# Kernel tuning notes

Measured on AMD Instinct MI355X. Metric: run time of the kernel, lower is better.

The kernel has to match this reference:

```python
import jax, jax.numpy as jnp
import numpy as np

NUM_LEVELS = 16
BASE_RES = 16
MAX_RES = 2048
TABLE_SIZE = 1 << 19
FEATS = 2
GROWTH = np.exp((np.log(MAX_RES) - np.log(BASE_RES)) / (NUM_LEVELS - 1))
SCALINGS = jnp.asarray(np.floor(BASE_RES * GROWTH ** np.arange(NUM_LEVELS)), dtype=jnp.float32)  # [L]
OFFSETS = jnp.arange(NUM_LEVELS, dtype=jnp.int32) * TABLE_SIZE  # per-level slice offset into table
AABB_MIN, AABB_MAX = -1.0, 1.0
P1, P2 = jnp.uint32(2654435761), jnp.uint32(805459861)
MASK = jnp.uint32(TABLE_SIZE - 1)


def sh16(d):
    # spherical harmonics components, levels=4 -> 16 components (nerfstudio convention)
    x, y, z = d[..., 0], d[..., 1], d[..., 2]
    xx, yy, zz = x * x, y * y, z * z
    return jnp.stack([
        jnp.full_like(x, 0.28209479177387814),
        -0.48860251190291987 * y,
        0.48860251190291987 * z,
        -0.48860251190291987 * x,
        1.0925484305920792 * x * y,
        -1.0925484305920792 * y * z,
        0.94617469575755997 * zz - 0.31539156525251999,
        -1.0925484305920792 * x * z,
        0.54627421529603959 * (xx - yy),
        0.59004358992664352 * y * (3.0 * xx - yy),
        2.8906114426405538 * x * y * z,
        0.45704579946446572 * y * (5.0 * zz - 1.0),
        0.37317633259011546 * z * (5.0 * zz - 3.0),
        0.45704579946446572 * x * (5.0 * zz - 1.0),
        1.4453057213202769 * z * (xx - yy),
        0.59004358992664352 * x * (xx - 3.0 * yy),
    ], axis=-1)


def hash_fn(x, y, z):
    # spatial hash with wraparound uint32 arithmetic; lower 19 bits match int64 math mod 2^19
    v = x ^ (y * P1) ^ (z * P2)
    return (v & MASK).astype(jnp.int32) + OFFSETS  # [N, L]


def hash_encode(pts, table):
    # pts: [N,3] in [0,1]; table: [L*T, F]
    scaled = pts[:, None, :] * SCALINGS[None, :, None]  # [N, L, 3]
    f = jnp.floor(scaled)
    c = jnp.ceil(scaled)
    off = scaled - f  # [N, L, 3]
    fi = f.astype(jnp.uint32)
    ci = c.astype(jnp.uint32)
    cx, cy, cz = ci[..., 0], ci[..., 1], ci[..., 2]
    fx, fy, fz = fi[..., 0], fi[..., 1], fi[..., 2]
    # corner order matches nerfstudio hashed_0..7
    idx = jnp.stack([
        hash_fn(cx, cy, cz), hash_fn(cx, fy, cz), hash_fn(fx, fy, cz), hash_fn(fx, cy, cz),
        hash_fn(cx, cy, fz), hash_fn(cx, fy, fz), hash_fn(fx, fy, fz), hash_fn(fx, cy, fz),
    ], axis=0)  # [8, N, L]
    feats = table[idx]  # [8, N, L, F]
    ox, oy, oz = off[..., 0:1], off[..., 1:2], off[..., 2:3]
    f03 = feats[0] * ox + feats[3] * (1.0 - ox)
    f12 = feats[1] * ox + feats[2] * (1.0 - ox)
    f56 = feats[5] * ox + feats[6] * (1.0 - ox)
    f47 = feats[4] * ox + feats[7] * (1.0 - ox)
    f0312 = f03 * oy + f12 * (1.0 - oy)
    f4756 = f47 * oy + f56 * (1.0 - oy)
    enc = f0312 * oz + f4756 * (1.0 - oz)  # [N, L, F]
    return enc.reshape(enc.shape[0], NUM_LEVELS * FEATS)


def setup_inputs() -> dict:
    key = jax.random.key(0)
    ks = jax.random.split(key, 16)
    B, S = 4096, 48
    positions = jax.random.uniform(ks[0], (B, S, 3), jnp.float32) * 2.0 - 1.0
    densities = jax.random.normal(ks[1], (B, S, 1), jnp.float32)
    normals = jax.random.normal(ks[2], (B, 3), jnp.float32)
    camera_to_worlds = jax.random.normal(ks[3], (B, 3, 4), jnp.float32) * 0.3
    hash_table = (jax.random.uniform(ks[4], (NUM_LEVELS * TABLE_SIZE, FEATS), jnp.float32) * 2.0 - 1.0) * 1e-4
    def lin(k, i, o):
        return jax.random.normal(k, (i, o), jnp.float32) * (1.0 / np.sqrt(i))
    return {
        'positions': positions, 'densities': densities, 'normals': normals,
        'camera_to_worlds': camera_to_worlds, 'hash_table': hash_table,
        'w1': lin(ks[5], 32, 64), 'b1': jnp.zeros((64,), jnp.float32),
        'w2': lin(ks[6], 64, 16), 'b2': jnp.zeros((16,), jnp.float32),
        'h1': lin(ks[7], 32, 64), 'hb1': jnp.zeros((64,), jnp.float32),
        'h2': lin(ks[8], 64, 64), 'hb2': jnp.zeros((64,), jnp.float32),
        'h3': lin(ks[9], 64, 3), 'hb3': jnp.zeros((3,), jnp.float32),
    }


def reference(positions, densities, normals, camera_to_worlds, hash_table,
              w1, b1, w2, b2, h1, hb1, h2, hb2, h3, hb3):
    B, S, _ = positions.shape
    R = camera_to_worlds[..., :3, :3]
    t = camera_to_worlds[..., :3, 3]
    Rinv = jnp.swapaxes(R, -1, -2)  # pose inverse for rigid transform
    tinv = -jnp.einsum('bij,bj->bi', Rinv, t)
    pos = jnp.einsum('bij,bsj->bsi', Rinv, positions) + tinv[:, None, :]  # world -> camera
    pos = (pos - AABB_MIN) / (AABB_MAX - AABB_MIN)  # SceneBox.get_normalized_positions
    n_cam = jnp.einsum('bij,bj->bi', Rinv, normals)
    n_cam = (n_cam + 1.0) / 2.0  # get_normalized_directions
    d = sh16(n_cam)  # [B, 16]
    d = jnp.broadcast_to(d[:, None, :], (B, S, 16)).reshape(-1, 16)
    selector = jnp.all((pos > 0.0) & (pos < 1.0), axis=-1)
    pos = pos * selector[..., None]
    enc = hash_encode(pos.reshape(-1, 3), hash_table)  # [B*S, 32]
    geo = jax.nn.relu(jax.nn.relu(enc @ w1 + b1) @ w2 + b2)  # mlp_base, out ReLU
    h = jnp.concatenate([d, geo], axis=-1)  # [B*S, 32]
    rgb = jax.nn.sigmoid(jax.nn.relu(jax.nn.relu(h @ h1 + hb1) @ h2 + hb2) @ h3 + hb3)
    rgb = rgb.reshape(B, S, 3)
    weight = jax.nn.softmax(densities, axis=-2)  # softmax over samples
    return jnp.sum(weight * rgb, axis=-2)  # [B, 3] == FieldHeadNames.RGB_AFFINE
```

## Files before the change

### kernel.cpp

```cpp
#include <hip/hip_runtime.h>
#include <math.h>
#include <stdint.h>

#define NLEV 16
#define TSIZE (1u << 19)
#define NB 4096
#define NS 48
#define NPTS (NB * NS)

typedef __attribute__((ext_vector_type(8))) short short8;
typedef __attribute__((ext_vector_type(4))) float f32x4;

struct Scales { float s[NLEV]; };

__device__ __forceinline__ uint32_t hash3(uint32_t x, uint32_t y, uint32_t z) {
    return (x ^ (y * 2654435761u) ^ (z * 805459861u)) & (TSIZE - 1u);
}

__device__ __forceinline__ float sigmoidf(float v) {
    return 1.0f / (1.0f + expf(-v));
}

__device__ __forceinline__ ushort f2b(float f) {
    union { float f; uint32_t u; } v; v.f = f;
    uint32_t r = (v.u + 0x7FFFu + ((v.u >> 16) & 1u)) >> 16;
    return (ushort)r;
}

#define MFMA16(a, b, c) __builtin_amdgcn_mfma_f32_16x16x32_bf16((a), (b), (c), 0, 0, 0)

__global__ __launch_bounds__(256) void prep_kernel(
    const float* __restrict__ w1, const float* __restrict__ w2,
    const float* __restrict__ h1, const float* __restrict__ h2,
    const float* __restrict__ h3,
    ushort* __restrict__ bank)
{
    for (int idx = threadIdx.x; idx < 20 * 512; idx += 256) {
        const int f    = idx >> 9;
        const int r    = idx & 511;
        const int lane = r >> 3;
        const int j    = r & 7;
        const int l15  = lane & 15;
        const int quad = lane >> 4;
        const int k8   = quad * 8 + j;
        float val;
        if (f < 4) {
            val = w1[k8 * 64 + f * 16 + l15];
        } else if (f < 6) {
            val = w2[((f - 4) * 32 + k8) * 16 + l15];
        } else if (f < 10) {
            val = h1[k8 * 64 + (f - 6) * 16 + l15];
        } else if (f < 18) {
            const int t = f - 10, nt = t >> 1, kk = t & 1;
            val = h2[(kk * 32 + k8) * 64 + nt * 16 + l15];
        } else {
            val = (l15 < 3) ? h3[((f - 18) * 32 + k8) * 3 + l15] : 0.0f;
        }
        bank[idx] = f2b(val);
    }
}

__global__ __launch_bounds__(256) void encode_kernel(
    const float* __restrict__ positions,
    const float* __restrict__ c2w,
    const float* __restrict__ table,
    uint32_t* __restrict__ enc_ws,
    Scales sc)
{
    const int p = blockIdx.x * blockDim.x + threadIdx.x;
    if (p >= NPTS) return;
    const int l = blockIdx.y;
    const int b = p / NS;

    const float* M = c2w + b * 12;
    const float px = positions[3 * p + 0];
    const float py = positions[3 * p + 1];
    const float pz = positions[3 * p + 2];
    const float dx = px - M[3], dy = py - M[7], dz = pz - M[11];
    float qx = M[0] * dx + M[4] * dy + M[8] * dz;
    float qy = M[1] * dx + M[5] * dy + M[9] * dz;
    float qz = M[2] * dx + M[6] * dy + M[10] * dz;
    qx = (qx + 1.0f) * 0.5f;
    qy = (qy + 1.0f) * 0.5f;
    qz = (qz + 1.0f) * 0.5f;
    const bool sel = (qx > 0.0f) && (qx < 1.0f) &&
                     (qy > 0.0f) && (qy < 1.0f) &&
                     (qz > 0.0f) && (qz < 1.0f);
    if (!sel) { qx = 0.0f; qy = 0.0f; qz = 0.0f; }

    const float s = sc.s[l];
    const float sx = qx * s, sy = qy * s, sz = qz * s;
    const float fx = floorf(sx), fy = floorf(sy), fz = floorf(sz);
    const float cx = ceilf(sx),  cy = ceilf(sy),  cz = ceilf(sz);
    const float ox = sx - fx, oy = sy - fy, oz = sz - fz;
    const uint32_t fxi = (uint32_t)fx, fyi = (uint32_t)fy, fzi = (uint32_t)fz;
    const uint32_t cxi = (uint32_t)cx, cyi = (uint32_t)cy, czi = (uint32_t)cz;

    const float2* tab2 = (const float2*)table + (uint32_t)l * TSIZE;
    const float2 f0 = tab2[hash3(cxi, cyi, czi)];
    const float2 f1 = tab2[hash3(cxi, fyi, czi)];
    const float2 f2 = tab2[hash3(fxi, fyi, czi)];
    const float2 f3 = tab2[hash3(fxi, cyi, czi)];
    const float2 f4 = tab2[hash3(cxi, cyi, fzi)];
    const float2 f5 = tab2[hash3(cxi, fyi, fzi)];
    const float2 f6 = tab2[hash3(fxi, fyi, fzi)];
    const float2 f7 = tab2[hash3(fxi, cyi, fzi)];

    const float omx = 1.0f - ox, omy = 1.0f - oy, omz = 1.0f - oz;
    float f03x = f0.x * ox + f3.x * omx, f03y = f0.y * ox + f3.y * omx;
    float f12x = f1.x * ox + f2.x * omx, f12y = f1.y * ox + f2.y * omx;
    float f56x = f5.x * ox + f6.x * omx, f56y = f5.y * ox + f6.y * omx;
    float f47x = f4.x * ox + f7.x * omx, f47y = f4.y * ox + f7.y * omx;
    float ax = f03x * oy + f12x * omy, ay = f03y * oy + f12y * omy;
    float bx = f47x * oy + f56x * omy, by = f47y * oy + f56y * omy;
    const float ex = ax * oz + bx * omz;
    const float ey = ay * oz + by * omz;
    enc_ws[l * NPTS + p] = ((uint32_t)f2b(ey) << 16) | (uint32_t)f2b(ex);
}

__global__ __launch_bounds__(256) void mfma_mlp_kernel(
    const uint32_t* __restrict__ enc_ws,
    const float* __restrict__ normals,
    const float* __restrict__ c2w,
    const ushort* __restrict__ bank,
    const float* __restrict__ b1, const float* __restrict__ b2,
    const float* __restrict__ hb1, const float* __restrict__ hb2,
    const float* __restrict__ hb3,
    float* __restrict__ rgb_out)
{
    __shared__ ushort sX[64 * 40];
    __shared__ ushort sA1[64 * 72];
    __shared__ ushort sHIN[64 * 40];
    __shared__ ushort sU[64 * 72];

    const int tid = threadIdx.x;
    const int p0  = blockIdx.x * 64;

    {
        const int pt = tid & 63;
        const int l0 = (tid >> 6) * 4;
        const int p  = p0 + pt;
#pragma unroll
        for (int l = l0; l < l0 + 4; ++l) {
            *(uint32_t*)&sX[pt * 40 + 2 * l] = enc_ws[l * NPTS + p];
        }
    }

    if (tid < 64) {
        const int p = p0 + tid;
        const int b = p / NS;
        const float* M = c2w + b * 12;
        const float n0 = normals[3 * b + 0];
        const float n1 = normals[3 * b + 1];
        const float n2 = normals[3 * b + 2];
        float x = M[0] * n0 + M[4] * n1 + M[8] * n2;
        float y = M[1] * n0 + M[5] * n1 + M[9] * n2;
        float z = M[2] * n0 + M[6] * n1 + M[10] * n2;
        x = (x + 1.0f) * 0.5f;
        y = (y + 1.0f) * 0.5f;
        z = (z + 1.0f) * 0.5f;
        const float xx = x * x, yy = y * y, zz = z * z;
        float sh[16];
        sh[0]  = 0.28209479177387814f;
        sh[1]  = -0.48860251190291987f * y;
        sh[2]  = 0.48860251190291987f * z;
        sh[3]  = -0.48860251190291987f * x;
        sh[4]  = 1.0925484305920792f * x * y;
        sh[5]  = -1.0925484305920792f * y * z;
        sh[6]  = 0.94617469575756f * zz - 0.31539156525252f;
        sh[7]  = -1.0925484305920792f * x * z;
        sh[8]  = 0.5462742152960396f * (xx - yy);
        sh[9]  = 0.5900435899266435f * y * (3.0f * xx - yy);
        sh[10] = 2.890611442640554f * x * y * z;
        sh[11] = 0.4570457994644657f * y * (5.0f * zz - 1.0f);
        sh[12] = 0.37317633259011546f * z * (5.0f * zz - 3.0f);
        sh[13] = 0.4570457994644657f * x * (5.0f * zz - 1.0f);
        sh[14] = 1.445305721320277f * z * (xx - yy);
        sh[15] = 0.5900435899266435f * x * (xx - 3.0f * yy);
#pragma unroll
        for (int i = 0; i < 16; ++i) sHIN[tid * 40 + i] = f2b(sh[i]);
    }

    const int lane = tid & 63;
    const int wv   = tid >> 6;
    const int l15  = lane & 15;
    const int quad = lane >> 4;
    float b1v[4], hb1v[4], hb2v[4];
#pragma unroll
    for (int nt = 0; nt < 4; ++nt) {
        b1v[nt]  = b1[nt * 16 + l15];
        hb1v[nt] = hb1[nt * 16 + l15];
        hb2v[nt] = hb2[nt * 16 + l15];
    }
    const float b2v  = b2[l15];
    const float hb3v = (l15 < 3) ? hb3[l15] : 0.0f;

    const ushort* fb = bank + lane * 8;
#define FRAG(f) (*(const short8*)(fb + (f) * 512))

    __syncthreads();

    const int arow  = wv * 16 + l15;
    const int crow0 = wv * 16 + quad * 4;
    const f32x4 zero = {0.0f, 0.0f, 0.0f, 0.0f};

    {
        const short8 a = *(const short8*)&sX[arow * 40 + quad * 8];
        f32x4 c[4];
#pragma unroll
        for (int nt = 0; nt < 4; ++nt) c[nt] = MFMA16(a, FRAG(nt), zero);
#pragma unroll
        for (int nt = 0; nt < 4; ++nt)
#pragma unroll
            for (int r = 0; r < 4; ++r) {
                const float v = fmaxf(c[nt][r] + b1v[nt], 0.0f);
                sA1[(crow0 + r) * 72 + nt * 16 + l15] = f2b(v);
            }
    }

    {
        const short8 a0 = *(const short8*)&sA1[arow * 72 + quad * 8];
        const short8 a1 = *(const short8*)&sA1[arow * 72 + 32 + quad * 8];
        f32x4 c = MFMA16(a0, FRAG(4), zero);
        c = MFMA16(a1, FRAG(5), c);
#pragma unroll
        for (int r = 0; r < 4; ++r) {
            const float v = fmaxf(c[r] + b2v, 0.0f);
            sHIN[(crow0 + r) * 40 + 16 + l15] = f2b(v);
        }
    }

    {
        const short8 a = *(const short8*)&sHIN[arow * 40 + quad * 8];
        f32x4 c[4];
#pragma unroll
        for (int nt = 0; nt < 4; ++nt) c[nt] = MFMA16(a, FRAG(6 + nt), zero);
#pragma unroll
        for (int nt = 0; nt < 4; ++nt)
#pragma unroll
            for (int r = 0; r < 4; ++r) {
                const float v = fmaxf(c[nt][r] + hb1v[nt], 0.0f);
                sU[(crow0 + r) * 72 + nt * 16 + l15] = f2b(v);
            }
    }

    {
        const short8 a0 = *(const short8*)&sU[arow * 72 + quad * 8];
        const short8 a1 = *(const short8*)&sU[arow * 72 + 32 + quad * 8];
        f32x4 c[4];
#pragma unroll
        for (int nt = 0; nt < 4; ++nt) {
            f32x4 t = MFMA16(a0, FRAG(10 + nt * 2), zero);
            c[nt] = MFMA16(a1, FRAG(11 + nt * 2), t);
        }
#pragma unroll
        for (int nt = 0; nt < 4; ++nt)
#pragma unroll
            for (int r = 0; r < 4; ++r) {
                const float v = fmaxf(c[nt][r] + hb2v[nt], 0.0f);
                sA1[(crow0 + r) * 72 + nt * 16 + l15] = f2b(v);
            }
    }

    {
        const short8 a0 = *(const short8*)&sA1[arow * 72 + quad * 8];
        const short8 a1 = *(const short8*)&sA1[arow * 72 + 32 + quad * 8];
        f32x4 c = MFMA16(a0, FRAG(18), zero);
        c = MFMA16(a1, FRAG(19), c);
        if (l15 < 3) {
#pragma unroll
            for (int r = 0; r < 4; ++r) {
                rgb_out[3 * (p0 + crow0 + r) + l15] = sigmoidf(c[r] + hb3v);
            }
        }
    }
#undef FRAG
}

__global__ __launch_bounds__(64) void reduce_kernel(
    const float* __restrict__ densities,
    const float* __restrict__ rgb,
    float* __restrict__ out)
{
    const int b = blockIdx.x;
    const int t = threadIdx.x;
    const bool valid = t < NS;

    float d = valid ? densities[b * NS + t] : -INFINITY;
    float m = d;
#pragma unroll
    for (int off = 32; off > 0; off >>= 1) m = fmaxf(m, __shfl_xor(m, off));
    float e = valid ? expf(d - m) : 0.0f;
    float sum = e;
#pragma unroll
    for (int off = 32; off > 0; off >>= 1) sum += __shfl_xor(sum, off);
    const float w = e / sum;

    float r0 = 0.0f, r1 = 0.0f, r2 = 0.0f;
    if (valid) {
        const int base = (b * NS + t) * 3;
        r0 = w * rgb[base + 0];
        r1 = w * rgb[base + 1];
        r2 = w * rgb[base + 2];
    }
#pragma unroll
    for (int off = 32; off > 0; off >>= 1) {
        r0 += __shfl_xor(r0, off);
        r1 += __shfl_xor(r1, off);
        r2 += __shfl_xor(r2, off);
    }
    if (t == 0) {
        out[3 * b + 0] = r0;
        out[3 * b + 1] = r1;
        out[3 * b + 2] = r2;
    }
}

extern "C" void kernel_launch(void* const* d_in, const int* in_sizes, int n_in,
                              void* d_out, int out_size, void* d_ws, size_t ws_size,
                              hipStream_t stream) {
    const float* positions = (const float*)d_in[0];
    const float* densities = (const float*)d_in[1];
    const float* normals   = (const float*)d_in[2];
    const float* c2w       = (const float*)d_in[3];
    const float* table     = (const float*)d_in[4];
    const float* w1  = (const float*)d_in[5];
    const float* b1  = (const float*)d_in[6];
    const float* w2  = (const float*)d_in[7];
    const float* b2  = (const float*)d_in[8];
    const float* h1  = (const float*)d_in[9];
    const float* hb1 = (const float*)d_in[10];
    const float* h2  = (const float*)d_in[11];
    const float* hb2 = (const float*)d_in[12];
    const float* h3  = (const float*)d_in[13];
    const float* hb3 = (const float*)d_in[14];
    float* out = (float*)d_out;

    ushort*   bank   = (ushort*)d_ws;
    uint32_t* enc_ws = (uint32_t*)((char*)d_ws + 20 * 1024);
    float*    rgb_ws = (float*)((char*)enc_ws + sizeof(uint32_t) * NLEV * NPTS);

    Scales sc;
    const double growth = exp((log(2048.0) - log(16.0)) / 15.0);
    for (int i = 0; i < NLEV; ++i)
        sc.s[i] = (float)floor(16.0 * pow(growth, (double)i));

    const int threads = 256;
    const int pblocks = NPTS / threads;

    prep_kernel<<<1, threads, 0, stream>>>(w1, w2, h1, h2, h3, bank);
    encode_kernel<<<dim3(pblocks, NLEV), threads, 0, stream>>>(
        positions, c2w, table, enc_ws, sc);
    mfma_mlp_kernel<<<NPTS / 64, threads, 0, stream>>>(
        enc_ws, normals, c2w, bank, b1, b2, hb1, hb2, hb3, rgb_ws);
    reduce_kernel<<<NB, 64, 0, stream>>>(densities, rgb_ws, out);
}
```

Measured before the change: 222.5 us.

## Fuse hash encoding into MLP kernel, dropping encoding workspace round-trip

Merges the per-level hash-grid encode kernel into the MFMA MLP kernel. Each block transforms its 64 points once into shared memory, then four waves each gather four levels and write packed bf16 features straight into the shared input tile. This removes the global write and re-read of the 16-level encoding buffer and one kernel launch. The cost is lower gather parallelism per block (4 levels per thread, run serially), fewer waves in flight to hide random table-lookup latency, and extra block-wide barriers between MLP stages.

Result: slower. 274.7 us (+23.4%).

```diff
diff --git a/kernel.cpp b/kernel.cpp
--- a/kernel.cpp
+++ b/kernel.cpp
@@ -60,74 +60,19 @@
     }
 }
 
-__global__ __launch_bounds__(256) void encode_kernel(
+__global__ __launch_bounds__(256) void fused_kernel(
     const float* __restrict__ positions,
+    const float* __restrict__ normals,
     const float* __restrict__ c2w,
     const float* __restrict__ table,
-    uint32_t* __restrict__ enc_ws,
-    Scales sc)
-{
-    const int p = blockIdx.x * blockDim.x + threadIdx.x;
-    if (p >= NPTS) return;
-    const int l = blockIdx.y;
-    const int b = p / NS;
-
-    const float* M = c2w + b * 12;
-    const float px = positions[3 * p + 0];
-    const float py = positions[3 * p + 1];
-    const float pz = positions[3 * p + 2];
-    const float dx = px - M[3], dy = py - M[7], dz = pz - M[11];
-    float qx = M[0] * dx + M[4] * dy + M[8] * dz;
-    float qy = M[1] * dx + M[5] * dy + M[9] * dz;
-    float qz = M[2] * dx + M[6] * dy + M[10] * dz;
-    qx = (qx + 1.0f) * 0.5f;
-    qy = (qy + 1.0f) * 0.5f;
-    qz = (qz + 1.0f) * 0.5f;
-    const bool sel = (qx > 0.0f) && (qx < 1.0f) &&
-                     (qy > 0.0f) && (qy < 1.0f) &&
-                     (qz > 0.0f) && (qz < 1.0f);
-    if (!sel) { qx = 0.0f; qy = 0.0f; qz = 0.0f; }
-
-    const float s = sc.s[l];
-    const float sx = qx * s, sy = qy * s, sz = qz * s;
-    const float fx = floorf(sx), fy = floorf(sy), fz = floorf(sz);
-    const float cx = ceilf(sx),  cy = ceilf(sy),  cz = ceilf(sz);
-    const float ox = sx - fx, oy = sy - fy, oz = sz - fz;
-    const uint32_t fxi = (uint32_t)fx, fyi = (uint32_t)fy, fzi = (uint32_t)fz;
-    const uint32_t cxi = (uint32_t)cx, cyi = (uint32_t)cy, czi = (uint32_t)cz;
-
-    const float2* tab2 = (const float2*)table + (uint32_t)l * TSIZE;
-    const float2 f0 = tab2[hash3(cxi, cyi, czi)];
-    const float2 f1 = tab2[hash3(cxi, fyi, czi)];
-    const float2 f2 = tab2[hash3(fxi, fyi, czi)];
-    const float2 f3 = tab2[hash3(fxi, cyi, czi)];
-    const float2 f4 = tab2[hash3(cxi, cyi, fzi)];
-    const float2 f5 = tab2[hash3(cxi, fyi, fzi)];
-    const float2 f6 = tab2[hash3(fxi, fyi, fzi)];
-    const float2 f7 = tab2[hash3(fxi, cyi, fzi)];
-
-    const float omx = 1.0f - ox, omy = 1.0f - oy, omz = 1.0f - oz;
-    float f03x = f0.x * ox + f3.x * omx, f03y = f0.y * ox + f3.y * omx;
-    float f12x = f1.x * ox + f2.x * omx, f12y = f1.y * ox + f2.y * omx;
-    float f56x = f5.x * ox + f6.x * omx, f56y = f5.y * ox + f6.y * omx;
-    float f47x = f4.x * ox + f7.x * omx, f47y = f4.y * ox + f7.y * omx;
-    float ax = f03x * oy + f12x * omy, ay = f03y * oy + f12y * omy;
-    float bx = f47x * oy + f56x * omy, by = f47y * oy + f56y * omy;
-    const float ex = ax * oz + bx * omz;
-    const float ey = ay * oz + by * omz;
-    enc_ws[l * NPTS + p] = ((uint32_t)f2b(ey) << 16) | (uint32_t)f2b(ex);
-}
-
-__global__ __launch_bounds__(256) void mfma_mlp_kernel(
-    const uint32_t* __restrict__ enc_ws,
-    const float* __restrict__ normals,
-    const float* __restrict__ c2w,
     const ushort* __restrict__ bank,
     const float* __restrict__ b1, const float* __restrict__ b2,
     const float* __restrict__ hb1, const float* __restrict__ hb2,
     const float* __restrict__ hb3,
-    float* __restrict__ rgb_out)
+    float* __restrict__ rgb_out,
+    Scales sc)
 {
+    __shared__ float4 sQ[64];
     __shared__ ushort sX[64 * 40];
     __shared__ ushort sA1[64 * 72];
     __shared__ ushort sHIN[64 * 40];
@@ -136,20 +81,26 @@
     const int tid = threadIdx.x;
     const int p0  = blockIdx.x * 64;
 
-    {
-        const int pt = tid & 63;
-        const int l0 = (tid >> 6) * 4;
-        const int p  = p0 + pt;
-#pragma unroll
-        for (int l = l0; l < l0 + 4; ++l) {
-            *(uint32_t*)&sX[pt * 40 + 2 * l] = enc_ws[l * NPTS + p];
-        }
-    }
-
     if (tid < 64) {
         const int p = p0 + tid;
         const int b = p / NS;
         const float* M = c2w + b * 12;
+        const float px = positions[3 * p + 0];
+        const float py = positions[3 * p + 1];
+        const float pz = positions[3 * p + 2];
+        const float dx = px - M[3], dy = py - M[7], dz = pz - M[11];
+        float qx = M[0] * dx + M[4] * dy + M[8] * dz;
+        float qy = M[1] * dx + M[5] * dy + M[9] * dz;
+        float qz = M[2] * dx + M[6] * dy + M[10] * dz;
+        qx = (qx + 1.0f) * 0.5f;
+        qy = (qy + 1.0f) * 0.5f;
+        qz = (qz + 1.0f) * 0.5f;
+        const bool sel = (qx > 0.0f) && (qx < 1.0f) &&
+                         (qy > 0.0f) && (qy < 1.0f) &&
+                         (qz > 0.0f) && (qz < 1.0f);
+        if (!sel) { qx = 0.0f; qy = 0.0f; qz = 0.0f; }
+        sQ[tid] = make_float4(qx, qy, qz, 0.0f);
+
         const float n0 = normals[3 * b + 0];
         const float n1 = normals[3 * b + 1];
         const float n2 = normals[3 * b + 2];
@@ -180,6 +131,46 @@
 #pragma unroll
         for (int i = 0; i < 16; ++i) sHIN[tid * 40 + i] = f2b(sh[i]);
     }
+    __syncthreads();
+
+    {
+        const int pt = tid & 63;
+        const int wv4 = tid >> 6;
+        const float4 q = sQ[pt];
+#pragma unroll
+        for (int i = 0; i < 4; ++i) {
+            const int l = i * 4 + wv4;
+            const float s = sc.s[l];
+            const float sx = q.x * s, sy = q.y * s, sz = q.z * s;
+            const float fx = floorf(sx), fy = floorf(sy), fz = floorf(sz);
+            const float cx = ceilf(sx),  cy = ceilf(sy),  cz = ceilf(sz);
+            const float ox = sx - fx, oy = sy - fy, oz = sz - fz;
+            const uint32_t fxi = (uint32_t)fx, fyi = (uint32_t)fy, fzi = (uint32_t)fz;
+            const uint32_t cxi = (uint32_t)cx, cyi = (uint32_t)cy, czi = (uint32_t)cz;
+
+            const float2* tab2 = (const float2*)table + (uint32_t)l * TSIZE;
+            const float2 f0 = tab2[hash3(cxi, cyi, czi)];
+            const float2 f1 = tab2[hash3(cxi, fyi, czi)];
+            const float2 f2 = tab2[hash3(fxi, fyi, czi)];
+            const float2 f3 = tab2[hash3(fxi, cyi, czi)];
+            const float2 f4 = tab2[hash3(cxi, cyi, fzi)];
+            const float2 f5 = tab2[hash3(cxi, fyi, fzi)];
+            const float2 f6 = tab2[hash3(fxi, fyi, fzi)];
+            const float2 f7 = tab2[hash3(fxi, cyi, fzi)];
+
+            const float omx = 1.0f - ox, omy = 1.0f - oy, omz = 1.0f - oz;
+            float f03x = f0.x * ox + f3.x * omx, f03y = f0.y * ox + f3.y * omx;
+            float f12x = f1.x * ox + f2.x * omx, f12y = f1.y * ox + f2.y * omx;
+            float f56x = f5.x * ox + f6.x * omx, f56y = f5.y * ox + f6.y * omx;
+            float f47x = f4.x * ox + f7.x * omx, f47y = f4.y * ox + f7.y * omx;
+            float ax = f03x * oy + f12x * omy, ay = f03y * oy + f12y * omy;
+            float bx = f47x * oy + f56x * omy, by = f47y * oy + f56y * omy;
+            const float ex = ax * oz + bx * omz;
+            const float ey = ay * oz + by * omz;
+            *(uint32_t*)&sX[pt * 40 + 2 * l] =
+                ((uint32_t)f2b(ey) << 16) | (uint32_t)f2b(ex);
+        }
+    }
 
     const int lane = tid & 63;
     const int wv   = tid >> 6;
@@ -217,6 +208,7 @@
                 sA1[(crow0 + r) * 72 + nt * 16 + l15] = f2b(v);
             }
     }
+    __syncthreads();
 
     {
         const short8 a0 = *(const short8*)&sA1[arow * 72 + quad * 8];
@@ -229,6 +221,7 @@
             sHIN[(crow0 + r) * 40 + 16 + l15] = f2b(v);
         }
     }
+    __syncthreads();
 
     {
         const short8 a = *(const short8*)&sHIN[arow * 40 + quad * 8];
@@ -243,6 +236,7 @@
                 sU[(crow0 + r) * 72 + nt * 16 + l15] = f2b(v);
             }
     }
+    __syncthreads();
 
     {
         const short8 a0 = *(const short8*)&sU[arow * 72 + quad * 8];
@@ -253,6 +247,7 @@
             f32x4 t = MFMA16(a0, FRAG(10 + nt * 2), zero);
             c[nt] = MFMA16(a1, FRAG(11 + nt * 2), t);
         }
+        __syncthreads();
 #pragma unroll
         for (int nt = 0; nt < 4; ++nt)
 #pragma unroll
@@ -261,6 +256,7 @@
                 sA1[(crow0 + r) * 72 + nt * 16 + l15] = f2b(v);
             }
     }
+    __syncthreads();
 
     {
         const short8 a0 = *(const short8*)&sA1[arow * 72 + quad * 8];
@@ -336,22 +332,17 @@
     const float* hb3 = (const float*)d_in[14];
     float* out = (float*)d_out;
 
-    ushort*   bank   = (ushort*)d_ws;
-    uint32_t* enc_ws = (uint32_t*)((char*)d_ws + 20 * 1024);
-    float*    rgb_ws = (float*)((char*)enc_ws + sizeof(uint32_t) * NLEV * NPTS);
+    ushort* bank   = (ushort*)d_ws;
+    float*  rgb_ws = (float*)((char*)d_ws + 20 * 1024);
 
     Scales sc;
     const double growth = exp((log(2048.0) - log(16.0)) / 15.0);
     for (int i = 0; i < NLEV; ++i)
         sc.s[i] = (float)floor(16.0 * pow(growth, (double)i));
 
-    const int threads = 256;
-    const int pblocks = NPTS / threads;
-
-    prep_kernel<<<1, threads, 0, stream>>>(w1, w2, h1, h2, h3, bank);
-    encode_kernel<<<dim3(pblocks, NLEV), threads, 0, stream>>>(
-        positions, c2w, table, enc_ws, sc);
-    mfma_mlp_kernel<<<NPTS / 64, threads, 0, stream>>>(
-        enc_ws, normals, c2w, bank, b1, b2, hb1, hb2, hb3, rgb_ws);
+    prep_kernel<<<1, 256, 0, stream>>>(w1, w2, h1, h2, h3, bank);
+    fused_kernel<<<NPTS / 64, 256, 0, stream>>>(
+        positions, normals, c2w, table, bank,
+        b1, b2, hb1, hb2, hb3, rgb_ws, sc);
     reduce_kernel<<<NB, 64, 0, stream>>>(densities, rgb_ws, out);
 }
```

## Convert hash table to packed bf16 and interleave levels in encode grid

Applied to the files above, without the earlier changes.

Adds a conversion pass in the prep kernel that packs the fp32 hash table into 4-byte bf16 pairs, then gathers from that smaller table in the encode kernel, halving the bytes per random gather. The encode grid is flattened so consecutive blocks cover different levels of the same points, which changes cache locality. Extra __syncthreads are inserted in the MLP kernel between shared-memory stages. The conversion reads and writes the whole 64 MB table on every call, which may cost more than the gathers save, and it reduces table precision.

After: 238.2 us. +7.0%, slower.

```diff
diff --git a/kernel.cpp b/kernel.cpp
--- a/kernel.cpp
+++ b/kernel.cpp
@@ -27,95 +27,153 @@
     return (ushort)r;
 }
 
+__device__ __forceinline__ float blo(uint32_t v) {
+    union { uint32_t u; float f; } t; t.u = v << 16; return t.f;
+}
+__device__ __forceinline__ float bhi(uint32_t v) {
+    union { uint32_t u; float f; } t; t.u = v & 0xFFFF0000u; return t.f;
+}
+
 #define MFMA16(a, b, c) __builtin_amdgcn_mfma_f32_16x16x32_bf16((a), (b), (c), 0, 0, 0)
 
 __global__ __launch_bounds__(256) void prep_kernel(
     const float* __restrict__ w1, const float* __restrict__ w2,
     const float* __restrict__ h1, const float* __restrict__ h2,
     const float* __restrict__ h3,
-    ushort* __restrict__ bank)
+    const float* __restrict__ table,
+    ushort* __restrict__ bank,
+    uint32_t* __restrict__ tb16)
 {
-    for (int idx = threadIdx.x; idx < 20 * 512; idx += 256) {
-        const int f    = idx >> 9;
-        const int r    = idx & 511;
-        const int lane = r >> 3;
-        const int j    = r & 7;
-        const int l15  = lane & 15;
-        const int quad = lane >> 4;
-        const int k8   = quad * 8 + j;
-        float val;
-        if (f < 4) {
-            val = w1[k8 * 64 + f * 16 + l15];
-        } else if (f < 6) {
-            val = w2[((f - 4) * 32 + k8) * 16 + l15];
-        } else if (f < 10) {
-            val = h1[k8 * 64 + (f - 6) * 16 + l15];
-        } else if (f < 18) {
-            const int t = f - 10, nt = t >> 1, kk = t & 1;
-            val = h2[(kk * 32 + k8) * 64 + nt * 16 + l15];
-        } else {
-            val = (l15 < 3) ? h3[((f - 18) * 32 + k8) * 3 + l15] : 0.0f;
-        }
-        bank[idx] = f2b(val);
-    }
-}
-
-__global__ __launch_bounds__(256) void encode_kernel(
+    if (blockIdx.x == 0) {
+        for (int idx = threadIdx.x; idx < 20 * 512; idx += 256) {
+            const int f    = idx >> 9;
+            const int r    = idx & 511;
+            const int lane = r >> 3;
+            const int j    = r & 7;
+            const int l15  = lane & 15;
+            const int quad = lane >> 4;
+            const int k8   = quad * 8 + j;
+            float val;
+            if (f < 4) {
+                val = w1[k8 * 64 + f * 16 + l15];
+            } else if (f < 6) {
+                val = w2[((f - 4) * 32 + k8) * 16 + l15];
+            } else if (f < 10) {
+                val = h1[k8 * 64 + (f - 6) * 16 + l15];
+            } else if (f < 18) {
+                const int t = f - 10, nt = t >> 1, kk = t & 1;
+                val = h2[(kk * 32 + k8) * 64 + nt * 16 + l15];
+            } else {
+                val = (l15 < 3) ? h3[((f - 18) * 32 + k8) * 3 + l15] : 0.0f;
+            }
+            bank[idx] = f2b(val);
+        }
+    }
+    if (tb16) {
+        const float2* t2 = (const float2*)table;
+        const int n = NLEV * TSIZE;
+        for (int i = blockIdx.x * blockDim.x + threadIdx.x; i < n;
+             i += gridDim.x * blockDim.x) {
+            const float2 e = t2[i];
+            tb16[i] = ((uint32_t)f2b(e.y) << 16) | (uint32_t)f2b(e.x);
+        }
+    }
+}
+
+#define ENCODE_PROLOG()                                                       \
+    const int bid = blockIdx.x;                                               \
+    const int l   = bid & 15;                         \
+    const int p   = (bid >> 4) * 256 + threadIdx.x;                           \
+    const int b   = p / NS;                                                   \
+    const float* M = c2w + b * 12;                                            \
+    const float px = positions[3 * p + 0];                                    \
+    const float py = positions[3 * p + 1];                                    \
+    const float pz = positions[3 * p + 2];                                    \
+    const float dx = px - M[3], dy = py - M[7], dz = pz - M[11];              \
+    float qx = M[0] * dx + M[4] * dy + M[8] * dz;                             \
+    float qy = M[1] * dx + M[5] * dy + M[9] * dz;                             \
+    float qz = M[2] * dx + M[6] * dy + M[10] * dz;                            \
+    qx = (qx + 1.0f) * 0.5f;                                                  \
+    qy = (qy + 1.0f) * 0.5f;                                                  \
+    qz = (qz + 1.0f) * 0.5f;                                                  \
+    const bool sel = (qx > 0.0f) && (qx < 1.0f) &&                            \
+                     (qy > 0.0f) && (qy < 1.0f) &&                            \
+                     (qz > 0.0f) && (qz < 1.0f);                              \
+    if (!sel) { qx = 0.0f; qy = 0.0f; qz = 0.0f; }                            \
+    const float s = sc.s[l];                                                  \
+    const float sx = qx * s, sy = qy * s, sz = qz * s;                        \
+    const float fx = floorf(sx), fy = floorf(sy), fz = floorf(sz);            \
+    const float cx = ceilf(sx),  cy = ceilf(sy),  cz = ceilf(sz);             \
+    const float ox = sx - fx, oy = sy - fy, oz = sz - fz;                     \
+    const uint32_t fxi = (uint32_t)fx, fyi = (uint32_t)fy, fzi = (uint32_t)fz;\
+    const uint32_t cxi = (uint32_t)cx, cyi = (uint32_t)cy, czi = (uint32_t)cz;
+
+#define ENCODE_EPILOG()                                                       \
+    const float omx = 1.0f - ox, omy = 1.0f - oy, omz = 1.0f - oz;            \
+    float f03x = f0x * ox + f3x * omx, f03y = f0y * ox + f3y * omx;           \
+    float f12x = f1x * ox + f2x * omx, f12y = f1y * ox + f2y * omx;           \
+    float f56x = f5x * ox + f6x * omx, f56y = f5y * ox + f6y * omx;           \
+    float f47x = f4x * ox + f7x * omx, f47y = f4y * ox + f7y * omx;           \
+    float ax = f03x * oy + f12x * omy, ay = f03y * oy + f12y * omy;           \
+    float bx = f47x * oy + f56x * omy, by = f47y * oy + f56y * omy;           \
+    const float ex = ax * oz + bx * omz;                                      \
+    const float ey = ay * oz + by * omz;                                      \
+    enc_ws[l * NPTS + p] = ((uint32_t)f2b(ey) << 16) | (uint32_t)f2b(ex);
+
+__global__ __launch_bounds__(256) void encode_kernel_b16(
+    const float* __restrict__ positions,
+    const float* __restrict__ c2w,
+    const uint32_t* __restrict__ tb16,
+    uint32_t* __restrict__ enc_ws,
+    Scales sc)
+{
+    ENCODE_PROLOG();
+    const uint32_t* tab = tb16 + (uint32_t)l * TSIZE;
+    const uint32_t e0 = tab[hash3(cxi, cyi, czi)];
+    const uint32_t e1 = tab[hash3(cxi, fyi, czi)];
+    const uint32_t e2 = tab[hash3(fxi, fyi, czi)];
+    const uint32_t e3 = tab[hash3(fxi, cyi, czi)];
+    const uint32_t e4 = tab[hash3(cxi, cyi, fzi)];
+    const uint32_t e5 = tab[hash3(cxi, fyi, fzi)];
+    const uint32_t e6 = tab[hash3(fxi, fyi, fzi)];
+    const uint32_t e7 = tab[hash3(fxi, cyi, fzi)];
+    const float f0x = blo(e0), f0y = bhi(e0);
+    const float f1x = blo(e1), f1y = bhi(e1);
+    const float f2x = blo(e2), f2y = bhi(e2);
+    const float f3x = blo(e3), f3y = bhi(e3);
+    const float f4x = blo(e4), f4y = bhi(e4);
+    const float f5x = blo(e5), f5y = bhi(e5);
+    const float f6x = blo(e6), f6y = bhi(e6);
+    const float f7x = blo(e7), f7y = bhi(e7);
+    ENCODE_EPILOG();
+}
+
+__global__ __launch_bounds__(256) void encode_kernel_f32(
     const float* __restrict__ positions,
     const float* __restrict__ c2w,
     const float* __restrict__ table,
     uint32_t* __restrict__ enc_ws,
     Scales sc)
 {
-    const int p = blockIdx.x * blockDim.x + threadIdx.x;
-    if (p >= NPTS) return;
-    const int l = blockIdx.y;
-    const int b = p / NS;
-
-    const float* M = c2w + b * 12;
-    const float px = positions[3 * p + 0];
-    const float py = positions[3 * p + 1];
-    const float pz = positions[3 * p + 2];
-    const float dx = px - M[3], dy = py - M[7], dz = pz - M[11];
-    float qx = M[0] * dx + M[4] * dy + M[8] * dz;
-    float qy = M[1] * dx + M[5] * dy + M[9] * dz;
-    float qz = M[2] * dx + M[6] * dy + M[10] * dz;
-    qx = (qx + 1.0f) * 0.5f;
-    qy = (qy + 1.0f) * 0.5f;
-    qz = (qz + 1.0f) * 0.5f;
-    const bool sel = (qx > 0.0f) && (qx < 1.0f) &&
-                     (qy > 0.0f) && (qy < 1.0f) &&
-                     (qz > 0.0f) && (qz < 1.0f);
-    if (!sel) { qx = 0.0f; qy = 0.0f; qz = 0.0f; }
-
-    const float s = sc.s[l];
-    const float sx = qx * s, sy = qy * s, sz = qz * s;
-    const float fx = floorf(sx), fy = floorf(sy), fz = floorf(sz);
-    const float cx = ceilf(sx),  cy = ceilf(sy),  cz = ceilf(sz);
-    const float ox = sx - fx, oy = sy - fy, oz = sz - fz;
-    const uint32_t fxi = (uint32_t)fx, fyi = (uint32_t)fy, fzi = (uint32_t)fz;
-    const uint32_t cxi = (uint32_t)cx, cyi = (uint32_t)cy, czi = (uint32_t)cz;
-
-    const float2* tab2 = (const float2*)table + (uint32_t)l * TSIZE;
-    const float2 f0 = tab2[hash3(cxi, cyi, czi)];
-    const float2 f1 = tab2[hash3(cxi, fyi, czi)];
-    const float2 f2 = tab2[hash3(fxi, fyi, czi)];
-    const float2 f3 = tab2[hash3(fxi, cyi, czi)];
-    const float2 f4 = tab2[hash3(cxi, cyi, fzi)];
-    const float2 f5 = tab2[hash3(cxi, fyi, fzi)];
-    const float2 f6 = tab2[hash3(fxi, fyi, fzi)];
-    const float2 f7 = tab2[hash3(fxi, cyi, fzi)];
-
-    const float omx = 1.0f - ox, omy = 1.0f - oy, omz = 1.0f - oz;
-    float f03x = f0.x * ox + f3.x * omx, f03y = f0.y * ox + f3.y * omx;
-    float f12x = f1.x * ox + f2.x * omx, f12y = f1.y * ox + f2.y * omx;
-    float f56x = f5.x * ox + f6.x * omx, f56y = f5.y * ox + f6.y * omx;
-    float f47x = f4.x * ox + f7.x * omx, f47y = f4.y * ox + f7.y * omx;
-    float ax = f03x * oy + f12x * omy, ay = f03y * oy + f12y * omy;
-    float bx = f47x * oy + f56x * omy, by = f47y * oy + f56y * omy;
-    const float ex = ax * oz + bx * omz;
-    const float ey = ay * oz + by * omz;
-    enc_ws[l * NPTS + p] = ((uint32_t)f2b(ey) << 16) | (uint32_t)f2b(ex);
+    ENCODE_PROLOG();
+    const float2* tab = (const float2*)table + (uint32_t)l * TSIZE;
+    const float2 g0 = tab[hash3(cxi, cyi, czi)];
+    const float2 g1 = tab[hash3(cxi, fyi, czi)];
+    const float2 g2 = tab[hash3(fxi, fyi, czi)];
+    const float2 g3 = tab[hash3(fxi, cyi, czi)];
+    const float2 g4 = tab[hash3(cxi, cyi, fzi)];
+    const float2 g5 = tab[hash3(cxi, fyi, fzi)];
+    const float2 g6 = tab[hash3(fxi, fyi, fzi)];
+    const float2 g7 = tab[hash3(fxi, cyi, fzi)];
+    const float f0x = g0.x, f0y = g0.y;
+    const float f1x = g1.x, f1y = g1.y;
+    const float f2x = g2.x, f2y = g2.y;
+    const float f3x = g3.x, f3y = g3.y;
+    const float f4x = g4.x, f4y = g4.y;
+    const float f5x = g5.x, f5y = g5.y;
+    const float f6x = g6.x, f6y = g6.y;
+    const float f7x = g7.x, f7y = g7.y;
+    ENCODE_EPILOG();
 }
 
 __global__ __launch_bounds__(256) void mfma_mlp_kernel(
@@ -217,6 +275,7 @@
                 sA1[(crow0 + r) * 72 + nt * 16 + l15] = f2b(v);
             }
     }
+    __syncthreads();
 
     {
         const short8 a0 = *(const short8*)&sA1[arow * 72 + quad * 8];
@@ -229,6 +288,7 @@
             sHIN[(crow0 + r) * 40 + 16 + l15] = f2b(v);
         }
     }
+    __syncthreads();
 
     {
         const short8 a = *(const short8*)&sHIN[arow * 40 + quad * 8];
@@ -243,6 +303,7 @@
                 sU[(crow0 + r) * 72 + nt * 16 + l15] = f2b(v);
             }
     }
+    __syncthreads();
 
     {
         const short8 a0 = *(const short8*)&sU[arow * 72 + quad * 8];
@@ -253,6 +314,7 @@
             f32x4 t = MFMA16(a0, FRAG(10 + nt * 2), zero);
             c[nt] = MFMA16(a1, FRAG(11 + nt * 2), t);
         }
+        __syncthreads();
 #pragma unroll
         for (int nt = 0; nt < 4; ++nt)
 #pragma unroll
@@ -261,6 +323,7 @@
                 sA1[(crow0 + r) * 72 + nt * 16 + l15] = f2b(v);
             }
     }
+    __syncthreads();
 
     {
         const short8 a0 = *(const short8*)&sA1[arow * 72 + quad * 8];
@@ -336,22 +399,32 @@
     const float* hb3 = (const float*)d_in[14];
     float* out = (float*)d_out;
 
-    ushort*   bank   = (ushort*)d_ws;
-    uint32_t* enc_ws = (uint32_t*)((char*)d_ws + 20 * 1024);
-    float*    rgb_ws = (float*)((char*)enc_ws + sizeof(uint32_t) * NLEV * NPTS);
+    const size_t BANK_B = 20 * 1024;
+    const size_t TB16_B = (size_t)NLEV * TSIZE * 4;
+    const size_t ENC_B  = (size_t)NLEV * NPTS * 4;
+    const size_t RGB_B  = (size_t)NPTS * 3 * 4;
+    const bool use_b16 = ws_size >= BANK_B + TB16_B + ENC_B + RGB_B;
+
+    ushort*   bank = (ushort*)d_ws;
+    uint32_t* tb16 = use_b16 ? (uint32_t*)((char*)d_ws + BANK_B) : nullptr;
+    char*     rest = (char*)d_ws + BANK_B + (use_b16 ? TB16_B : 0);
+    uint32_t* enc_ws = (uint32_t*)rest;
+    float*    rgb_ws = (float*)(rest + ENC_B);
 
     Scales sc;
     const double growth = exp((log(2048.0) - log(16.0)) / 15.0);
     for (int i = 0; i < NLEV; ++i)
         sc.s[i] = (float)floor(16.0 * pow(growth, (double)i));
 
-    const int threads = 256;
-    const int pblocks = NPTS / threads;
-
-    prep_kernel<<<1, threads, 0, stream>>>(w1, w2, h1, h2, h3, bank);
-    encode_kernel<<<dim3(pblocks, NLEV), threads, 0, stream>>>(
-        positions, c2w, table, enc_ws, sc);
-    mfma_mlp_kernel<<<NPTS / 64, threads, 0, stream>>>(
+    prep_kernel<<<4096, 256, 0, stream>>>(w1, w2, h1, h2, h3, table, bank, tb16);
+    if (use_b16) {
+        encode_kernel_b16<<<(NPTS / 256) * NLEV, 256, 0, stream>>>(
+            positions, c2w, tb16, enc_ws, sc);
+    } else {
+        encode_kernel_f32<<<(NPTS / 256) * NLEV, 256, 0, stream>>>(
+            positions, c2w, table, enc_ws, sc);
+    }
+    mfma_mlp_kernel<<<NPTS / 64, 256, 0, stream>>>(
         enc_ws, normals, c2w, bank, b1, b2, hb1, hb2, hb3, rgb_ws);
     reduce_kernel<<<NB, 64, 0, stream>>>(densities, rgb_ws, out);
 }
```
